# Kernel optimization log

Hardware: AMD Instinct MI355X
Metric: run time of the kernel (lower is better)

## Reference

```python
import jax, jax.numpy as jnp
import numpy as np

NTYPES = 4
RCUT = 6.0
MIXED_TYPES = False
BOX = 40.0  # Angstrom, sets realistic atomic density


def setup_inputs() -> dict:
    key = jax.random.key(0)
    k1, k2 = jax.random.split(key)
    nframes, nloc = 2, 4096
    coord = jax.random.uniform(k1, (nframes, nloc * 3), dtype=jnp.float32) * BOX
    atype = jax.random.randint(k2, (nframes, nloc), 0, NTYPES, dtype=jnp.int32)
    return {"coord": coord, "atype": atype}


def reference(coord, atype):
    # cell=None branch: extended coords == local coords, nall == nloc
    nframes = coord.shape[0]
    c = coord.reshape(nframes, -1, 3)              # (f, nloc, 3)
    nloc = c.shape[1]
    # diff[f, i, j] = coord[j] - coord[i], shape (f, nloc, nall, 3)
    diff = c[:, None, :, :] - c[:, :, None, :]
    rr2 = jnp.sum(diff * diff, axis=-1)            # (f, nloc, nall)
    # mask self-pairs with inf (torch sets diff rows to inf before squaring)
    eye = jnp.eye(nloc, dtype=bool)
    rr2 = jnp.where(eye[None, :, :], jnp.inf, rr2)
    min_rr2 = jnp.min(rr2, axis=-1)                # (f, nloc)
    mask = rr2 < RCUT ** 2                         # (f, nloc, nall)
    if not MIXED_TYPES:
        # per-type neighbor counts via one-hot contraction (replaces the
        # Python loop over ntypes in the torch code; same math)
        onehot = jax.nn.one_hot(atype, NTYPES, dtype=jnp.int32)  # (f, nall, t)
        nnei = jnp.einsum('fij,fjt->fit', mask.astype(jnp.int32), onehot)
    else:
        valid = (atype >= 0)[:, None, :]
        nnei = jnp.sum(mask & valid, axis=-1).astype(jnp.int32)[..., None]
    max_nnei = jnp.max(nnei, axis=1)               # (f, ntypes) or (f, 1)
    return min_rr2, max_nnei
```

## Files before the change

kernel.cpp:

```cpp
#include <hip/hip_runtime.h>
#include <stdint.h>

#define NFRAMES 2
#define NT 4
#define BLK 256
#define NJ 64
#define JT 64
#define IPT 2
#define FBLK 64

template <bool SELFCHK>
__device__ __forceinline__ void do_pair(float cx, float cy, float cz, unsigned sval,
                                        int j, int i,
                                        float xi, float yi, float zi,
                                        float& mm, unsigned& cc) {
#pragma clang fp contract(off)
    float dx = cx - xi;
    float dy = cy - yi;
    float dz = cz - zi;
    float xx = dx * dx;
    float yy = dy * dy;
    float zz = dz * dz;
    float r2 = (xx + yy) + zz;
    bool self = SELFCHK && (j == i);
    mm = fminf(mm, self ? __builtin_inff() : r2);
    bool near = (r2 < 36.0f) && !self;
    cc += near ? sval : 0u;
}

template <bool SELFCHK>
__device__ __forceinline__ void tile_loop(const float4* __restrict__ sj, int jbase,
                                          const int (&ii)[IPT],
                                          const float (&xi)[IPT],
                                          const float (&yi)[IPT],
                                          const float (&zi)[IPT],
                                          float (&mA)[IPT], float (&mB)[IPT],
                                          unsigned (&cA)[IPT], unsigned (&cB)[IPT]) {
#pragma unroll 8
    for (int l = 0; l < JT; l += 2) {
        float4 c0 = sj[l];
        float4 c1 = sj[l + 1];
        const unsigned s0 = __float_as_uint(c0.w);
        const unsigned s1 = __float_as_uint(c1.w);
        const int j0 = jbase + l;
#pragma unroll
        for (int k = 0; k < IPT; ++k)
            do_pair<SELFCHK>(c0.x, c0.y, c0.z, s0, j0, ii[k], xi[k], yi[k], zi[k], mA[k], cA[k]);
#pragma unroll
        for (int k = 0; k < IPT; ++k)
            do_pair<SELFCHK>(c1.x, c1.y, c1.z, s1, j0 + 1, ii[k], xi[k], yi[k], zi[k], mB[k], cB[k]);
    }
}

__global__ __launch_bounds__(BLK) void ns_pair_kernel(const float* __restrict__ coord,
                                                      const int* __restrict__ atype,
                                                      uint2* __restrict__ part,
                                                      float* __restrict__ out,
                                                      int nloc) {
    const int f = blockIdx.z;
    const int q = nloc / IPT;
    const int ib = blockIdx.y * BLK;
    const int jbase = blockIdx.x * JT;

    if (blockIdx.x == 0 && blockIdx.y == 0 && f == 0 && threadIdx.x < NFRAMES * NT)
        ((unsigned*)out)[(size_t)NFRAMES * nloc + threadIdx.x] = 0u;

    const float* cf = coord + (size_t)f * nloc * 3;
    const int*   tf = atype + (size_t)f * nloc;

    __shared__ float4 sj[JT];
    if (threadIdx.x < JT) {
        const int jl = jbase + threadIdx.x;
        sj[threadIdx.x] = make_float4(cf[3 * jl], cf[3 * jl + 1], cf[3 * jl + 2],
                                      __uint_as_float(1u << (tf[jl] * 8)));
    }
    __syncthreads();

    int ii[IPT];
    float xi[IPT], yi[IPT], zi[IPT];
    float mA[IPT], mB[IPT];
    unsigned cA[IPT], cB[IPT];
    bool ov = false;
#pragma unroll
    for (int k = 0; k < IPT; ++k) {
        const int base = ib + k * q;
        ii[k] = base + threadIdx.x;
        xi[k] = cf[3 * ii[k]];
        yi[k] = cf[3 * ii[k] + 1];
        zi[k] = cf[3 * ii[k] + 2];
        mA[k] = mB[k] = __builtin_inff();
        cA[k] = cB[k] = 0u;
        ov |= (jbase >= base) && (jbase < base + BLK);
    }

    if (ov)
        tile_loop<true >(sj, jbase, ii, xi, yi, zi, mA, mB, cA, cB);
    else
        tile_loop<false>(sj, jbase, ii, xi, yi, zi, mA, mB, cA, cB);

    const size_t pb = ((size_t)blockIdx.x * NFRAMES + f) * nloc;
#pragma unroll
    for (int k = 0; k < IPT; ++k)
        part[pb + ii[k]] = make_uint2(__float_as_uint(fminf(mA[k], mB[k])), cA[k] + cB[k]);
}

__global__ __launch_bounds__(FBLK) void ns_finalize_kernel(const uint2* __restrict__ part,
                                                           float* __restrict__ out,
                                                           int nloc) {
    const int nbpf = nloc / FBLK;
    const int f = blockIdx.x / nbpf;
    const int i = (blockIdx.x % nbpf) * FBLK + threadIdx.x;

    float ma = __builtin_inff(), mb = __builtin_inff();
    unsigned cacc = 0u, cbacc = 0u;
#pragma unroll 16
    for (int jb = 0; jb < NJ; jb += 2) {
        uint2 va = part[((size_t)jb * NFRAMES + f) * nloc + i];
        uint2 vb = part[((size_t)(jb + 1) * NFRAMES + f) * nloc + i];
        ma = fminf(ma, __uint_as_float(va.x));
        mb = fminf(mb, __uint_as_float(vb.x));
        cacc += va.y;
        cbacc += vb.y;
    }
    out[(size_t)f * nloc + i] = fminf(ma, mb);
    const unsigned c = cacc + cbacc;

    int m0 = (int)(c & 255u);
    int m1 = (int)((c >> 8) & 255u);
    int m2 = (int)((c >> 16) & 255u);
    int m3 = (int)(c >> 24);
    for (int off = 32; off > 0; off >>= 1) {
        m0 = max(m0, __shfl_xor(m0, off, 64));
        m1 = max(m1, __shfl_xor(m1, off, 64));
        m2 = max(m2, __shfl_xor(m2, off, 64));
        m3 = max(m3, __shfl_xor(m3, off, 64));
    }
    if (threadIdx.x < NT) {
        const int t = threadIdx.x;
        const int mv = (t == 0) ? m0 : (t == 1) ? m1 : (t == 2) ? m2 : m3;
        atomicMax((unsigned*)out + (size_t)NFRAMES * nloc + f * NT + t,
                  __float_as_uint((float)mv));
    }
}

extern "C" void kernel_launch(void* const* d_in, const int* in_sizes, int n_in,
                              void* d_out, int out_size, void* d_ws, size_t ws_size,
                              hipStream_t stream) {
    const float* coord = (const float*)d_in[0];
    const int*   atype = (const int*)d_in[1];
    const int nloc = in_sizes[1] / NFRAMES;

    float* out  = (float*)d_out;
    uint2* part = (uint2*)d_ws;

    dim3 grid(NJ, nloc / (BLK * IPT), NFRAMES);
    ns_pair_kernel<<<grid, dim3(BLK), 0, stream>>>(coord, atype, part, out, nloc);

    const int nbpf = nloc / FBLK;
    ns_finalize_kernel<<<NFRAMES * nbpf, FBLK, 0, stream>>>(part, out, nloc);
}
```

Baseline: 24.89 us.

## Vectorize pair distance with packed f32x2 FMA and SoA shared tiles

The j-tile in shared memory changes from AoS float4 to separate x/y/z/type arrays so that two j atoms can be read as packed f32x2 vectors. Distances are then computed with packed subtract/mul/FMA, aiming for the MI355X packed FP32 instructions to halve the VALU work per pair. The j tile shrinks to 32 and the number of j blocks doubles to 128, which raises grid parallelism but also doubles the partial buffer the finalize pass must reduce. Using FMA also changes the rounding of r2 compared with the reference's separate multiply and add, which could flip borderline cutoff comparisons.

```diff
diff --git a/kernel.cpp b/kernel.cpp
--- a/kernel.cpp
+++ b/kernel.cpp
@@ -4,51 +4,46 @@
 #define NFRAMES 2
 #define NT 4
 #define BLK 256
-#define NJ 64
-#define JT 64
+#define NJ 128
+#define JT 32
 #define IPT 2
 #define FBLK 64
 
-template <bool SELFCHK>
-__device__ __forceinline__ void do_pair(float cx, float cy, float cz, unsigned sval,
-                                        int j, int i,
-                                        float xi, float yi, float zi,
-                                        float& mm, unsigned& cc) {
-#pragma clang fp contract(off)
-    float dx = cx - xi;
-    float dy = cy - yi;
-    float dz = cz - zi;
-    float xx = dx * dx;
-    float yy = dy * dy;
-    float zz = dz * dz;
-    float r2 = (xx + yy) + zz;
-    bool self = SELFCHK && (j == i);
-    mm = fminf(mm, self ? __builtin_inff() : r2);
-    bool near = (r2 < 36.0f) && !self;
-    cc += near ? sval : 0u;
-}
+typedef float f32x2 __attribute__((ext_vector_type(2)));
 
 template <bool SELFCHK>
-__device__ __forceinline__ void tile_loop(const float4* __restrict__ sj, int jbase,
+__device__ __forceinline__ void tile_loop(const f32x2* __restrict__ px,
+                                          const f32x2* __restrict__ py,
+                                          const f32x2* __restrict__ pz,
+                                          const uint2* __restrict__ ps,
+                                          int jbase,
                                           const int (&ii)[IPT],
-                                          const float (&xi)[IPT],
-                                          const float (&yi)[IPT],
-                                          const float (&zi)[IPT],
-                                          float (&mA)[IPT], float (&mB)[IPT],
+                                          const f32x2 (&Xi)[IPT],
+                                          const f32x2 (&Yi)[IPT],
+                                          const f32x2 (&Zi)[IPT],
+                                          float (&mm)[IPT],
                                           unsigned (&cA)[IPT], unsigned (&cB)[IPT]) {
-#pragma unroll 8
-    for (int l = 0; l < JT; l += 2) {
-        float4 c0 = sj[l];
-        float4 c1 = sj[l + 1];
-        const unsigned s0 = __float_as_uint(c0.w);
-        const unsigned s1 = __float_as_uint(c1.w);
-        const int j0 = jbase + l;
 #pragma unroll
-        for (int k = 0; k < IPT; ++k)
-            do_pair<SELFCHK>(c0.x, c0.y, c0.z, s0, j0, ii[k], xi[k], yi[k], zi[k], mA[k], cA[k]);
+    for (int h = 0; h < JT / 2; ++h) {
+        const f32x2 jx = px[h], jy = py[h], jz = pz[h];
+        const uint2 s2 = ps[h];
+        const int j0 = jbase + 2 * h;
 #pragma unroll
-        for (int k = 0; k < IPT; ++k)
-            do_pair<SELFCHK>(c1.x, c1.y, c1.z, s1, j0 + 1, ii[k], xi[k], yi[k], zi[k], mB[k], cB[k]);
+        for (int k = 0; k < IPT; ++k) {
+            f32x2 dx = jx - Xi[k];
+            f32x2 dy = jy - Yi[k];
+            f32x2 dz = jz - Zi[k];
+            f32x2 zz = dz * dz;
+            f32x2 t  = __builtin_elementwise_fma(dy, dy, zz);
+            f32x2 r2 = __builtin_elementwise_fma(dx, dx, t);
+            if (SELFCHK) {
+                r2.x = (j0     == ii[k]) ? __builtin_inff() : r2.x;
+                r2.y = (j0 + 1 == ii[k]) ? __builtin_inff() : r2.y;
+            }
+            mm[k] = fminf(mm[k], fminf(r2.x, r2.y));
+            cA[k] += (r2.x < 36.0f) ? s2.x : 0u;
+            cB[k] += (r2.y < 36.0f) ? s2.y : 0u;
+        }
     }
 }
 
@@ -68,40 +63,49 @@
     const float* cf = coord + (size_t)f * nloc * 3;
     const int*   tf = atype + (size_t)f * nloc;
 
-    __shared__ float4 sj[JT];
+    __shared__ float    sx[JT], sy[JT], sz[JT];
+    __shared__ unsigned st[JT];
     if (threadIdx.x < JT) {
         const int jl = jbase + threadIdx.x;
-        sj[threadIdx.x] = make_float4(cf[3 * jl], cf[3 * jl + 1], cf[3 * jl + 2],
-                                      __uint_as_float(1u << (tf[jl] * 8)));
+        sx[threadIdx.x] = cf[3 * jl];
+        sy[threadIdx.x] = cf[3 * jl + 1];
+        sz[threadIdx.x] = cf[3 * jl + 2];
+        st[threadIdx.x] = 1u << (tf[jl] * 8);
     }
     __syncthreads();
 
     int ii[IPT];
-    float xi[IPT], yi[IPT], zi[IPT];
-    float mA[IPT], mB[IPT];
+    f32x2 Xi[IPT], Yi[IPT], Zi[IPT];
+    float mm[IPT];
     unsigned cA[IPT], cB[IPT];
     bool ov = false;
 #pragma unroll
     for (int k = 0; k < IPT; ++k) {
         const int base = ib + k * q;
         ii[k] = base + threadIdx.x;
-        xi[k] = cf[3 * ii[k]];
-        yi[k] = cf[3 * ii[k] + 1];
-        zi[k] = cf[3 * ii[k] + 2];
-        mA[k] = mB[k] = __builtin_inff();
+        const float x = cf[3 * ii[k]], y = cf[3 * ii[k] + 1], z = cf[3 * ii[k] + 2];
+        Xi[k] = (f32x2){x, x};
+        Yi[k] = (f32x2){y, y};
+        Zi[k] = (f32x2){z, z};
+        mm[k] = __builtin_inff();
         cA[k] = cB[k] = 0u;
         ov |= (jbase >= base) && (jbase < base + BLK);
     }
 
+    const f32x2* px = (const f32x2*)sx;
+    const f32x2* py = (const f32x2*)sy;
+    const f32x2* pz = (const f32x2*)sz;
+    const uint2* ps = (const uint2*)st;
+
     if (ov)
-        tile_loop<true >(sj, jbase, ii, xi, yi, zi, mA, mB, cA, cB);
+        tile_loop<true >(px, py, pz, ps, jbase, ii, Xi, Yi, Zi, mm, cA, cB);
     else
-        tile_loop<false>(sj, jbase, ii, xi, yi, zi, mA, mB, cA, cB);
+        tile_loop<false>(px, py, pz, ps, jbase, ii, Xi, Yi, Zi, mm, cA, cB);
 
     const size_t pb = ((size_t)blockIdx.x * NFRAMES + f) * nloc;
 #pragma unroll
     for (int k = 0; k < IPT; ++k)
-        part[pb + ii[k]] = make_uint2(__float_as_uint(fminf(mA[k], mB[k])), cA[k] + cB[k]);
+        part[pb + ii[k]] = make_uint2(__float_as_uint(mm[k]), cA[k] + cB[k]);
 }
 
 __global__ __launch_bounds__(FBLK) void ns_finalize_kernel(const uint2* __restrict__ part,
```

Measured after the change: 28.03 us. +12.6%, slower.
